# Optimization experiments

Hardware: AMD Instinct MI355X
Metric: run time of the kernel (lower is better)

The kernel has to match this reference:

```python
import jax, jax.numpy as jnp
import numpy as np

N, E, B = 20000, 160000, 64
NFEAT, NHID, HEADS, NCLASS = 128, 64, 16, 10
GAT_SLOPE = 0.2    # LeakyReLU inside GATv2 attention
OUT_SLOPE = 0.01   # torch.nn.functional.leaky_relu default
TEMPERATURE = 1.0


def _lrelu(x, slope):
    return jnp.where(x >= 0, x, slope * x)


def gatv2_conv(x, src, dst, Wl, bl, Wr, br, att, bias):
    # x: [N, Fin]; PyG GATv2Conv with share_weights=False, concat=False (mean over heads)
    xl = (x @ Wl + bl).reshape(N, HEADS, NHID)   # source-side transform
    xr = (x @ Wr + br).reshape(N, HEADS, NHID)   # target-side transform
    e = _lrelu(xl[src] + xr[dst], GAT_SLOPE)     # [E', H, C] per-edge pre-activation
    logit = jnp.einsum('ehc,hc->eh', e, att)     # [E', H]
    # segment softmax over incoming edges of each target node (self-loops guarantee >=1 edge)
    m = jax.ops.segment_max(logit, dst, num_segments=N)
    m = jnp.where(jnp.isfinite(m), m, 0.0)
    ex = jnp.exp(logit - m[dst])
    den = jax.ops.segment_sum(ex, dst, num_segments=N)
    alpha = ex / den[dst]                        # [E', H]
    out = jax.ops.segment_sum(alpha[:, :, None] * xl[src], dst, num_segments=N)  # [N, H, C]
    return out.mean(axis=1) + bias               # concat=False -> head average, then bias


def setup_inputs() -> dict:
    key = jax.random.key(0)
    ks = jax.random.split(key, 20)
    s = 0.05
    inp = {
        'x': jax.random.normal(ks[0], (N, NFEAT), dtype=jnp.float32),
        'edge_index': jax.random.randint(ks[1], (2, E), 0, N, dtype=jnp.int64)
            if jax.config.jax_enable_x64 else jax.random.randint(ks[1], (2, E), 0, N).astype(jnp.int32),
        'batch': jnp.sort(jax.random.randint(ks[2], (N,), 0, B)).astype(jnp.int32),
        # GATv2 layer 1
        'W1l': jax.random.normal(ks[3], (NFEAT, HEADS * NHID), dtype=jnp.float32) * s,
        'b1l': jnp.zeros((HEADS * NHID,), jnp.float32),
        'W1r': jax.random.normal(ks[4], (NFEAT, HEADS * NHID), dtype=jnp.float32) * s,
        'b1r': jnp.zeros((HEADS * NHID,), jnp.float32),
        'att1': jax.random.normal(ks[5], (HEADS, NHID), dtype=jnp.float32) * s,
        'bias1': jnp.zeros((NHID,), jnp.float32),
        # GATv2 layer 2
        'W2l': jax.random.normal(ks[6], (NHID, HEADS * NHID), dtype=jnp.float32) * s,
        'b2l': jnp.zeros((HEADS * NHID,), jnp.float32),
        'W2r': jax.random.normal(ks[7], (NHID, HEADS * NHID), dtype=jnp.float32) * s,
        'b2r': jnp.zeros((HEADS * NHID,), jnp.float32),
        'att2': jax.random.normal(ks[8], (HEADS, NHID), dtype=jnp.float32) * s,
        'bias2': jnp.zeros((NHID,), jnp.float32),
        # heads
        'Wc': jax.random.normal(ks[9], (NHID, NCLASS), dtype=jnp.float32) * s,
        'bc': jnp.zeros((NCLASS,), jnp.float32),
        'Wv': jax.random.normal(ks[10], (NHID, 1), dtype=jnp.float32) * s,
        'bv': jnp.zeros((1,), jnp.float32),
    }
    return inp


def reference(x, edge_index, batch, W1l, b1l, W1r, b1r, att1, bias1,
              W2l, b2l, W2r, b2r, att2, bias2, Wc, bc, Wv, bv):
    loop = jnp.arange(N, dtype=edge_index.dtype)  # PyG add_self_loops=True
    src = jnp.concatenate([edge_index[0], loop])
    dst = jnp.concatenate([edge_index[1], loop])

    h = _lrelu(gatv2_conv(x, src, dst, W1l, b1l, W1r, b1r, att1, bias1), OUT_SLOPE)
    h = _lrelu(gatv2_conv(h, src, dst, W2l, b2l, W2r, b2r, att2, bias2), OUT_SLOPE)
    # dropout p=0.0 -> identity

    sums = jax.ops.segment_sum(h, batch, num_segments=B)           # [B, NHID]
    cnt = jax.ops.segment_sum(jnp.ones((N,), h.dtype), batch, num_segments=B)
    pooled = sums / jnp.maximum(cnt, 1.0)[:, None]                 # global_mean_pool

    logits = (pooled @ Wc + bc) / TEMPERATURE                      # [B, NCLASS]
    log_var = pooled @ Wv + bv                                     # [B, 1]
    return (logits, log_var)
```

## Files before the change

### kernel.cpp

```cpp
#include <hip/hip_runtime.h>
#include <hip/hip_bf16.h>
#include <hip/hip_fp16.h>
#include <math.h>

#define NN   20000
#define EE   160000
#define NBAT 64
#define NF   128
#define NH   64
#define NHEAD 16
#define NCLS 10
#define ETOT (EE + NN)

typedef __attribute__((ext_vector_type(8))) short short8;
typedef __attribute__((ext_vector_type(8))) _Float16 half8;
typedef __attribute__((ext_vector_type(4))) float f32x4;
typedef unsigned short ushort_t;

static __device__ __forceinline__ ushort_t f2bf_rn(float x) {
    unsigned u = __builtin_bit_cast(unsigned, x);
    unsigned r = (u + 0x7fffu + ((u >> 16) & 1u)) >> 16;
    return (ushort_t)r;
}
static __device__ __forceinline__ float bf2f(ushort_t u) {
    unsigned v = (unsigned)u << 16;
    return __builtin_bit_cast(float, v);
}

__global__ void k_init_deg(int* __restrict__ deg) {
    int n = blockIdx.x * 256 + threadIdx.x;
    if (n < NN) deg[n] = 1;
}

__global__ void k_hist(const int* __restrict__ ei, int* __restrict__ deg) {
    int e = blockIdx.x * 256 + threadIdx.x;
    if (e < EE) atomicAdd(&deg[ei[EE + e]], 1);
}

__global__ void k_scan(const int* __restrict__ deg, int* __restrict__ rowptr,
                       int* __restrict__ cursor) {
    const int T = 1024, PER = (NN + T - 1) / T;
    __shared__ int part[T];
    int t = threadIdx.x;
    int local[PER];
    int s = 0;
    #pragma unroll
    for (int i = 0; i < PER; ++i) {
        int idx = t * PER + i;
        int v = (idx < NN) ? deg[idx] : 0;
        local[i] = v; s += v;
    }
    part[t] = s;
    __syncthreads();
    for (int off = 1; off < T; off <<= 1) {
        int v = (t >= off) ? part[t - off] : 0;
        __syncthreads();
        part[t] += v;
        __syncthreads();
    }
    int ex = (t == 0) ? 0 : part[t - 1];
    #pragma unroll
    for (int i = 0; i < PER; ++i) {
        int idx = t * PER + i;
        if (idx < NN) { rowptr[idx] = ex; cursor[idx] = ex; ex += local[i]; }
    }
    if (t == T - 1) rowptr[NN] = ex;
}

__global__ void k_scatter(const int* __restrict__ ei, int* __restrict__ cursor,
                          int* __restrict__ csr) {
    int e = blockIdx.x * 256 + threadIdx.x;
    if (e >= ETOT) return;
    int s, d;
    if (e < EE) { s = ei[e]; d = ei[EE + e]; }
    else        { s = e - EE; d = s; }
    int pos = atomicAdd(&cursor[d], 1);
    csr[pos] = s;
}

__global__ void k_bounds(const int* __restrict__ batch, int* __restrict__ bstart) {
    int n = blockIdx.x * 256 + threadIdx.x;
    if (n >= NN) return;
    int b = batch[n];
    if (n == 0) for (int bb = 0; bb <= b; ++bb) bstart[bb] = 0;
    int bn = (n + 1 < NN) ? batch[n + 1] : NBAT;
    for (int bb = b + 1; bb <= bn; ++bb) bstart[bb] = n + 1;
}

__global__ void k_split_a(const float* __restrict__ A, ushort_t* __restrict__ hi,
                          ushort_t* __restrict__ lo, int count4) {
    int idx = blockIdx.x * 256 + threadIdx.x;
    if (idx >= count4) return;
    float4 x = *(const float4*)(A + idx * 4);
    ushort4 h, l;
    h.x = f2bf_rn(x.x); l.x = f2bf_rn(x.x - bf2f(h.x));
    h.y = f2bf_rn(x.y); l.y = f2bf_rn(x.y - bf2f(h.y));
    h.z = f2bf_rn(x.z); l.z = f2bf_rn(x.z - bf2f(h.z));
    h.w = f2bf_rn(x.w); l.w = f2bf_rn(x.w - bf2f(h.w));
    *(ushort4*)(hi + idx * 4) = h;
    *(ushort4*)(lo + idx * 4) = l;
}

template<int K>
__global__ void k_split_w(const float* __restrict__ W, ushort_t* __restrict__ hi,
                          ushort_t* __restrict__ lo) {
    int idx = blockIdx.x * 256 + threadIdx.x;
    if (idx >= K * 1024) return;
    int k = idx >> 10, n = idx & 1023;
    float x = W[idx];
    ushort_t h = f2bf_rn(x);
    hi[n * K + k] = h;
    lo[n * K + k] = f2bf_rn(x - bf2f(h));
}

template<int K>
__global__ __launch_bounds__(256) void k_gemm_mfma(
    const ushort_t* __restrict__ Ahi, const ushort_t* __restrict__ Alo, int M,
    const ushort_t* __restrict__ W0hi, const ushort_t* __restrict__ W0lo,
    const float* __restrict__ b0, _Float16* __restrict__ O0,
    const ushort_t* __restrict__ W1hi, const ushort_t* __restrict__ W1lo,
    const float* __restrict__ b1, _Float16* __restrict__ O1)
{
    const ushort_t* Whi = blockIdx.z ? W1hi : W0hi;
    const ushort_t* Wlo = blockIdx.z ? W1lo : W0lo;
    const float*    bi  = blockIdx.z ? b1 : b0;
    _Float16*       O   = blockIdx.z ? O1 : O0;

    const int r0 = blockIdx.x * 128;
    const int c0 = blockIdx.y * 128;

    __shared__ __align__(16) ushort_t As_hi[128 * 64];
    __shared__ __align__(16) ushort_t As_lo[128 * 64];
    __shared__ __align__(16) ushort_t Ws_hi[128 * 64];
    __shared__ __align__(16) ushort_t Ws_lo[128 * 64];

    const int t = threadIdx.x;
    const int lane = t & 63;
    const int wv = t >> 6, wr = wv >> 1, wc = wv & 1;
    const int fr = lane & 15;
    const int k0 = (lane >> 4) * 8;

    f32x4 acc[4][4] = {};

    for (int kt = 0; kt < K; kt += 64) {
        #pragma unroll
        for (int p = 0; p < 4; ++p) {
            int idx = p * 256 + t;
            int m  = idx >> 3;
            int kc = (idx & 7) * 8;
            int gr = r0 + m;
            uint4 vh = make_uint4(0, 0, 0, 0), vl = make_uint4(0, 0, 0, 0);
            if (gr < M) {
                vh = *(const uint4*)(Ahi + (size_t)gr * K + kt + kc);
                vl = *(const uint4*)(Alo + (size_t)gr * K + kt + kc);
            }
            int sw = (m * 128 + kc * 2) ^ ((m & 7) << 4);
            *(uint4*)((char*)As_hi + sw) = vh;
            *(uint4*)((char*)As_lo + sw) = vl;
            uint4 wh = *(const uint4*)(Whi + (size_t)(c0 + m) * K + kt + kc);
            uint4 wl = *(const uint4*)(Wlo + (size_t)(c0 + m) * K + kt + kc);
            *(uint4*)((char*)Ws_hi + sw) = wh;
            *(uint4*)((char*)Ws_lo + sw) = wl;
        }
        __syncthreads();

        #pragma unroll
        for (int ks = 0; ks < 64; ks += 32) {
            short8 ah[4], al[4], bh[4], bl[4];
            #pragma unroll
            for (int i = 0; i < 4; ++i) {
                int row = wr * 64 + i * 16 + fr;
                int off = (row * 128 + (ks + k0) * 2) ^ ((row & 7) << 4);
                ah[i] = *(const short8*)((const char*)As_hi + off);
                al[i] = *(const short8*)((const char*)As_lo + off);
            }
            #pragma unroll
            for (int j = 0; j < 4; ++j) {
                int col = wc * 64 + j * 16 + fr;
                int off = (col * 128 + (ks + k0) * 2) ^ ((col & 7) << 4);
                bh[j] = *(const short8*)((const char*)Ws_hi + off);
                bl[j] = *(const short8*)((const char*)Ws_lo + off);
            }
            #pragma unroll
            for (int i = 0; i < 4; ++i)
                #pragma unroll
                for (int j = 0; j < 4; ++j) {
                    acc[i][j] = __builtin_amdgcn_mfma_f32_16x16x32_bf16(ah[i], bh[j], acc[i][j], 0, 0, 0);
                    acc[i][j] = __builtin_amdgcn_mfma_f32_16x16x32_bf16(ah[i], bl[j], acc[i][j], 0, 0, 0);
                    acc[i][j] = __builtin_amdgcn_mfma_f32_16x16x32_bf16(al[i], bh[j], acc[i][j], 0, 0, 0);
                }
        }
        __syncthreads();
    }

    float bj[4];
    #pragma unroll
    for (int j = 0; j < 4; ++j) bj[j] = bi[c0 + wc * 64 + j * 16 + fr];
    #pragma unroll
    for (int i = 0; i < 4; ++i) {
        int rbase = r0 + wr * 64 + i * 16 + (lane >> 4) * 4;
        #pragma unroll
        for (int r = 0; r < 4; ++r) {
            int gr = rbase + r;
            if (gr < M) {
                #pragma unroll
                for (int j = 0; j < 4; ++j)
                    O[(size_t)gr * 1024 + c0 + wc * 64 + j * 16 + fr] =
                        (_Float16)(acc[i][j][r] + bj[j]);
            }
        }
    }
}

template<int SPLIT>
__global__ __launch_bounds__(256) void k_attn(
    const _Float16* __restrict__ xl, const _Float16* __restrict__ xr,
    const float* __restrict__ att, const float* __restrict__ bias,
    const int* __restrict__ rowptr, const int* __restrict__ csr,
    float* __restrict__ hout, ushort_t* __restrict__ hhi, ushort_t* __restrict__ hlo)
{
    const int wave = threadIdx.x >> 6;
    const int lane = threadIdx.x & 63;
    const int n = blockIdx.x * 4 + wave;
    if (n >= NN) return;
    const int h  = lane >> 2;
    const int cc = lane & 3;
    const int cb = h * NH + cc * 16;

    float attv[16], xrv[16], acc[16];
    #pragma unroll
    for (int i = 0; i < 4; ++i)
        *(float4*)(attv + i * 4) = *(const float4*)(att + cb + i * 4);
    {
        half8 q0 = *(const half8*)(xr + (size_t)n * 1024 + cb);
        half8 q1 = *(const half8*)(xr + (size_t)n * 1024 + cb + 8);
        #pragma unroll
        for (int j = 0; j < 8; ++j) { xrv[j] = (float)q0[j]; xrv[8 + j] = (float)q1[j]; }
    }
    #pragma unroll
    for (int j = 0; j < 16; ++j) acc[j] = 0.f;

    float m = -INFINITY, den = 0.f;
    const int e0 = rowptr[n], e1 = rowptr[n + 1];
    int e = e0;

    for (; e + 2 <= e1; e += 2) {
        const int s0 = csr[e], s1 = csr[e + 1];
        const _Float16* p0 = xl + (size_t)s0 * 1024 + cb;
        const _Float16* p1 = xl + (size_t)s1 * 1024 + cb;
        half8 a0 = *(const half8*)p0;
        half8 a1 = *(const half8*)(p0 + 8);
        half8 b0 = *(const half8*)p1;
        half8 b1 = *(const half8*)(p1 + 8);
        float x0[16], x1[16];
        #pragma unroll
        for (int j = 0; j < 8; ++j) {
            x0[j] = (float)a0[j]; x0[8 + j] = (float)a1[j];
            x1[j] = (float)b0[j]; x1[8 + j] = (float)b1[j];
        }
        float l0 = 0.f, l1 = 0.f;
        #pragma unroll
        for (int j = 0; j < 16; ++j) {
            float t0 = x0[j] + xrv[j];
            float t1 = x1[j] + xrv[j];
            t0 = fmaxf(t0, 0.2f * t0);
            t1 = fmaxf(t1, 0.2f * t1);
            l0 = fmaf(t0, attv[j], l0);
            l1 = fmaf(t1, attv[j], l1);
        }
        l0 += __shfl_xor(l0, 1); l1 += __shfl_xor(l1, 1);
        l0 += __shfl_xor(l0, 2); l1 += __shfl_xor(l1, 2);
        {
            const float nm = fmaxf(m, l0);
            const float p  = __expf(l0 - nm);
            const float sc = __expf(m - nm);
            den = den * sc + p;
            #pragma unroll
            for (int j = 0; j < 16; ++j) acc[j] = fmaf(acc[j], sc, p * x0[j]);
            m = nm;
        }
        {
            const float nm = fmaxf(m, l1);
            const float p  = __expf(l1 - nm);
            const float sc = __expf(m - nm);
            den = den * sc + p;
            #pragma unroll
            for (int j = 0; j < 16; ++j) acc[j] = fmaf(acc[j], sc, p * x1[j]);
            m = nm;
        }
    }
    for (; e < e1; ++e) {
        const int s = csr[e];
        const _Float16* p0 = xl + (size_t)s * 1024 + cb;
        half8 a0 = *(const half8*)p0;
        half8 a1 = *(const half8*)(p0 + 8);
        float x0[16];
        #pragma unroll
        for (int j = 0; j < 8; ++j) { x0[j] = (float)a0[j]; x0[8 + j] = (float)a1[j]; }
        float l0 = 0.f;
        #pragma unroll
        for (int j = 0; j < 16; ++j) {
            float t0 = x0[j] + xrv[j];
            t0 = fmaxf(t0, 0.2f * t0);
            l0 = fmaf(t0, attv[j], l0);
        }
        l0 += __shfl_xor(l0, 1);
        l0 += __shfl_xor(l0, 2);
        const float nm = fmaxf(m, l0);
        const float p  = __expf(l0 - nm);
        const float sc = __expf(m - nm);
        den = den * sc + p;
        #pragma unroll
        for (int j = 0; j < 16; ++j) acc[j] = fmaf(acc[j], sc, p * x0[j]);
        m = nm;
    }

    const float inv = 1.f / den;
    float v[16];
    #pragma unroll
    for (int j = 0; j < 16; ++j) v[j] = acc[j] * inv;
    #pragma unroll
    for (int mask = 4; mask <= 32; mask <<= 1)
        #pragma unroll
        for (int j = 0; j < 16; ++j) v[j] += __shfl_xor(v[j], mask);

    if (h == 0) {
        float bvv[16];
        #pragma unroll
        for (int i = 0; i < 4; ++i)
            *(float4*)(bvv + i * 4) = *(const float4*)(bias + cc * 16 + i * 4);
        #pragma unroll
        for (int i = 0; i < 4; ++i) {
            float o[4];
            #pragma unroll
            for (int r = 0; r < 4; ++r) {
                float tt = v[i * 4 + r] * 0.0625f + bvv[i * 4 + r];
                o[r] = fmaxf(tt, 0.01f * tt);
            }
            if (SPLIT) {
                ushort4 hh, ll;
                hh.x = f2bf_rn(o[0]); ll.x = f2bf_rn(o[0] - bf2f(hh.x));
                hh.y = f2bf_rn(o[1]); ll.y = f2bf_rn(o[1] - bf2f(hh.y));
                hh.z = f2bf_rn(o[2]); ll.z = f2bf_rn(o[2] - bf2f(hh.z));
                hh.w = f2bf_rn(o[3]); ll.w = f2bf_rn(o[3] - bf2f(hh.w));
                *(ushort4*)(hhi + (size_t)n * NH + cc * 16 + i * 4) = hh;
                *(ushort4*)(hlo + (size_t)n * NH + cc * 16 + i * 4) = ll;
            } else {
                *(float4*)(hout + (size_t)n * NH + cc * 16 + i * 4) =
                    make_float4(o[0], o[1], o[2], o[3]);
            }
        }
    }
}

#define PNODES 128
__global__ __launch_bounds__(256) void k_pool_partial(
    const float* __restrict__ h2, const int* __restrict__ batch,
    float* __restrict__ sums)
{
    const int n0 = blockIdx.x * PNODES;
    const int c = threadIdx.x & 63;
    const int r = threadIdx.x >> 6;
    const int nend = (n0 + PNODES < NN) ? n0 + PNODES : NN;
    float s = 0.f;
    int bcur = -1;
    for (int n = n0 + r; n < nend; n += 4) {
        int b = batch[n];
        if (b != bcur) {
            if (bcur >= 0) atomicAdd(&sums[bcur * NH + c], s);
            bcur = b; s = 0.f;
        }
        s += h2[(size_t)n * NH + c];
    }
    if (bcur >= 0) atomicAdd(&sums[bcur * NH + c], s);
}

__global__ void k_heads(const float* __restrict__ sums, const int* __restrict__ bstart,
                        const float* __restrict__ Wc, const float* __restrict__ bc,
                        const float* __restrict__ Wv, const float* __restrict__ bv,
                        float* __restrict__ out)
{
    const int b = blockIdx.x, c = threadIdx.x;
    const float cnt = (float)(bstart[b + 1] - bstart[b]);
    const float pooled = sums[b * NH + c] / fmaxf(cnt, 1.f);
    __shared__ float pl[NH];
    pl[c] = pooled;
    __syncthreads();
    if (c < NCLS) {
        float a = bc[c];
        for (int k = 0; k < NH; ++k) a = fmaf(pl[k], Wc[k * NCLS + c], a);
        out[b * NCLS + c] = a;
    } else if (c == NCLS) {
        float a = bv[0];
        for (int k = 0; k < NH; ++k) a = fmaf(pl[k], Wv[k], a);
        out[NBAT * NCLS + b] = a;
    }
}

extern "C" void kernel_launch(void* const* d_in, const int* in_sizes, int n_in,
                              void* d_out, int out_size, void* d_ws, size_t ws_size,
                              hipStream_t stream)
{
    const float* x     = (const float*)d_in[0];
    const int*   ei    = (const int*)  d_in[1];
    const int*   batch = (const int*)  d_in[2];
    const float* W1l = (const float*)d_in[3],  *b1l = (const float*)d_in[4];
    const float* W1r = (const float*)d_in[5],  *b1r = (const float*)d_in[6];
    const float* att1 = (const float*)d_in[7], *bias1 = (const float*)d_in[8];
    const float* W2l = (const float*)d_in[9],  *b2l = (const float*)d_in[10];
    const float* W2r = (const float*)d_in[11], *b2r = (const float*)d_in[12];
    const float* att2 = (const float*)d_in[13], *bias2 = (const float*)d_in[14];
    const float* Wc = (const float*)d_in[15],  *bc = (const float*)d_in[16];
    const float* Wv = (const float*)d_in[17],  *bv = (const float*)d_in[18];
    float* out = (float*)d_out;

    char* ws = (char*)d_ws;
    size_t off = 0;
    auto carve = [&](size_t bytes) {
        char* p = ws + off;
        off = (off + bytes + 255) & ~(size_t)255;
        return p;
    };
    _Float16* xl    = (_Float16*)carve((size_t)NN * 1024 * 2);
    _Float16* xr    = (_Float16*)carve((size_t)NN * 1024 * 2);
    float*    h2    = (float*)carve((size_t)NN * NH * 4);
    float*    psums = (float*)carve((size_t)NBAT * NH * 4);
    ushort_t* Axhi  = (ushort_t*)carve((size_t)NN * NF * 2);
    ushort_t* Axlo  = (ushort_t*)carve((size_t)NN * NF * 2);
    ushort_t* h1hi  = (ushort_t*)carve((size_t)NN * NH * 2);
    ushort_t* h1lo  = (ushort_t*)carve((size_t)NN * NH * 2);
    ushort_t* Wt1lh = (ushort_t*)carve((size_t)1024 * NF * 2);
    ushort_t* Wt1ll = (ushort_t*)carve((size_t)1024 * NF * 2);
    ushort_t* Wt1rh = (ushort_t*)carve((size_t)1024 * NF * 2);
    ushort_t* Wt1rl = (ushort_t*)carve((size_t)1024 * NF * 2);
    ushort_t* Wt2lh = (ushort_t*)carve((size_t)1024 * NH * 2);
    ushort_t* Wt2ll = (ushort_t*)carve((size_t)1024 * NH * 2);
    ushort_t* Wt2rh = (ushort_t*)carve((size_t)1024 * NH * 2);
    ushort_t* Wt2rl = (ushort_t*)carve((size_t)1024 * NH * 2);
    int*      deg    = (int*)carve((size_t)NN * 4);
    int*      cursor = (int*)carve((size_t)NN * 4);
    int*      rowptr = (int*)carve((size_t)(NN + 1) * 4);
    int*      csr    = (int*)carve((size_t)ETOT * 4);
    int*      bstart = (int*)carve((size_t)(NBAT + 1) * 4);

    k_init_deg<<<(NN + 255) / 256, 256, 0, stream>>>(deg);
    k_hist   <<<(EE + 255) / 256, 256, 0, stream>>>(ei, deg);
    k_scan   <<<1, 1024, 0, stream>>>(deg, rowptr, cursor);
    k_scatter<<<(ETOT + 255) / 256, 256, 0, stream>>>(ei, cursor, csr);
    k_bounds <<<(NN + 255) / 256, 256, 0, stream>>>(batch, bstart);

    k_split_a<<<(NN * NF / 4 + 255) / 256, 256, 0, stream>>>(x, Axhi, Axlo, NN * NF / 4);
    k_split_w<NF><<<(NF * 1024 + 255) / 256, 256, 0, stream>>>(W1l, Wt1lh, Wt1ll);
    k_split_w<NF><<<(NF * 1024 + 255) / 256, 256, 0, stream>>>(W1r, Wt1rh, Wt1rl);
    k_split_w<NH><<<(NH * 1024 + 255) / 256, 256, 0, stream>>>(W2l, Wt2lh, Wt2ll);
    k_split_w<NH><<<(NH * 1024 + 255) / 256, 256, 0, stream>>>(W2r, Wt2rh, Wt2rl);

    const int MB = (NN + 127) / 128;
    k_gemm_mfma<NF><<<dim3(MB, 8, 2), 256, 0, stream>>>(
        Axhi, Axlo, NN, Wt1lh, Wt1ll, b1l, xl, Wt1rh, Wt1rl, b1r, xr);
    k_attn<1><<<NN / 4, 256, 0, stream>>>(xl, xr, att1, bias1, rowptr, csr,
                                          (float*)nullptr, h1hi, h1lo);
    k_gemm_mfma<NH><<<dim3(MB, 8, 2), 256, 0, stream>>>(
        h1hi, h1lo, NN, Wt2lh, Wt2ll, b2l, xl, Wt2rh, Wt2rl, b2r, xr);
    k_attn<0><<<NN / 4, 256, 0, stream>>>(xl, xr, att2, bias2, rowptr, csr,
                                          h2, (ushort_t*)nullptr, (ushort_t*)nullptr);
    hipMemsetAsync(psums, 0, (size_t)NBAT * NH * 4, stream);
    k_pool_partial<<<(NN + PNODES - 1) / PNODES, 256, 0, stream>>>(h2, batch, psums);
    k_heads<<<NBAT, NH, 0, stream>>>(psums, bstart, Wc, bc, Wv, bv, out);
}
```

Baseline: 387.1 us.

## Use packed fp16 dot2 in attention, unroll edges by four, restructure CSR build

The attention logit is now computed in packed fp16 (add, leaky-relu, fdot2 against fp16 attention weights) instead of converting every gathered element to fp32. The edge loop is unrolled to four gathers per iteration so more loads are in flight. Self-loops are written directly in the scan kernel, and the degree init kernel is replaced by a memset. The GEMM grid is swapped so column tiles vary fastest, which may improve reuse of the A tile in cache. The fp16 arithmetic lowers logit precision, which risks accuracy drift.

```diff
diff --git a/kernel.cpp b/kernel.cpp
--- a/kernel.cpp
+++ b/kernel.cpp
@@ -14,8 +14,21 @@
 
 typedef __attribute__((ext_vector_type(8))) short short8;
 typedef __attribute__((ext_vector_type(8))) _Float16 half8;
+typedef __attribute__((ext_vector_type(2))) _Float16 h2;
 typedef __attribute__((ext_vector_type(4))) float f32x4;
 typedef unsigned short ushort_t;
+
+#if __has_builtin(__builtin_amdgcn_fdot2)
+typedef __fp16 fdot2_t __attribute__((ext_vector_type(2)));
+static __device__ __forceinline__ float dot2(h2 a, h2 b, float c) {
+    return __builtin_amdgcn_fdot2(__builtin_bit_cast(fdot2_t, a),
+                                  __builtin_bit_cast(fdot2_t, b), c, false);
+}
+#else
+static __device__ __forceinline__ float dot2(h2 a, h2 b, float c) {
+    return c + (float)a.x * (float)b.x + (float)a.y * (float)b.y;
+}
+#endif
 
 static __device__ __forceinline__ ushort_t f2bf_rn(float x) {
     unsigned u = __builtin_bit_cast(unsigned, x);
@@ -27,18 +40,13 @@
     return __builtin_bit_cast(float, v);
 }
 
-__global__ void k_init_deg(int* __restrict__ deg) {
-    int n = blockIdx.x * 256 + threadIdx.x;
-    if (n < NN) deg[n] = 1;
-}
-
 __global__ void k_hist(const int* __restrict__ ei, int* __restrict__ deg) {
     int e = blockIdx.x * 256 + threadIdx.x;
     if (e < EE) atomicAdd(&deg[ei[EE + e]], 1);
 }
 
 __global__ void k_scan(const int* __restrict__ deg, int* __restrict__ rowptr,
-                       int* __restrict__ cursor) {
+                       int* __restrict__ cursor, int* __restrict__ csr) {
     const int T = 1024, PER = (NN + T - 1) / T;
     __shared__ int part[T];
     int t = threadIdx.x;
@@ -62,18 +70,22 @@
     #pragma unroll
     for (int i = 0; i < PER; ++i) {
         int idx = t * PER + i;
-        if (idx < NN) { rowptr[idx] = ex; cursor[idx] = ex; ex += local[i]; }
-    }
-    if (t == T - 1) rowptr[NN] = ex;
+        if (idx < NN) {
+            int base = ex + idx;
+            rowptr[idx] = base;
+            csr[base]   = idx;
+            cursor[idx] = base + 1;
+            ex += local[i];
+        }
+    }
+    if (t == T - 1) rowptr[NN] = ex + NN;
 }
 
 __global__ void k_scatter(const int* __restrict__ ei, int* __restrict__ cursor,
                           int* __restrict__ csr) {
     int e = blockIdx.x * 256 + threadIdx.x;
-    if (e >= ETOT) return;
-    int s, d;
-    if (e < EE) { s = ei[e]; d = ei[EE + e]; }
-    else        { s = e - EE; d = s; }
+    if (e >= EE) return;
+    int s = ei[e], d = ei[EE + e];
     int pos = atomicAdd(&cursor[d], 1);
     csr[pos] = s;
 }
@@ -126,8 +138,8 @@
     const float*    bi  = blockIdx.z ? b1 : b0;
     _Float16*       O   = blockIdx.z ? O1 : O0;
 
-    const int r0 = blockIdx.x * 128;
-    const int c0 = blockIdx.y * 128;
+    const int c0 = blockIdx.x * 128;
+    const int r0 = blockIdx.y * 128;
 
     __shared__ __align__(16) ushort_t As_hi[128 * 64];
     __shared__ __align__(16) ushort_t As_lo[128 * 64];
@@ -212,6 +224,36 @@
     }
 }
 
+static __device__ __forceinline__ void edge_update(
+    half8 a0, half8 a1, half8 xr0, half8 xr1, const h2* att2,
+    float& m, float& den, float* acc)
+{
+    half8 t0 = a0 + xr0;
+    half8 t1 = a1 + xr1;
+    t0 = __builtin_elementwise_max(t0, t0 * (_Float16)0.2f);
+    t1 = __builtin_elementwise_max(t1, t1 * (_Float16)0.2f);
+    const h2* p0 = (const h2*)&t0;
+    const h2* p1 = (const h2*)&t1;
+    float lg = 0.f;
+    #pragma unroll
+    for (int j = 0; j < 4; ++j) lg = dot2(p0[j], att2[j], lg);
+    #pragma unroll
+    for (int j = 0; j < 4; ++j) lg = dot2(p1[j], att2[4 + j], lg);
+    lg += __shfl_xor(lg, 1);
+    lg += __shfl_xor(lg, 2);
+    const float nm = fmaxf(m, lg);
+    const float p  = __expf(lg - nm);
+    const float sc = __expf(m - nm);
+    den = den * sc + p;
+    const _Float16* xa = (const _Float16*)&a0;
+    const _Float16* xb = (const _Float16*)&a1;
+    #pragma unroll
+    for (int j = 0; j < 8; ++j) acc[j]     = fmaf((float)xa[j], p, acc[j] * sc);
+    #pragma unroll
+    for (int j = 0; j < 8; ++j) acc[8 + j] = fmaf((float)xb[j], p, acc[8 + j] * sc);
+    m = nm;
+}
+
 template<int SPLIT>
 __global__ __launch_bounds__(256) void k_attn(
     const _Float16* __restrict__ xl, const _Float16* __restrict__ xr,
@@ -227,92 +269,43 @@
     const int cc = lane & 3;
     const int cb = h * NH + cc * 16;
 
-    float attv[16], xrv[16], acc[16];
-    #pragma unroll
-    for (int i = 0; i < 4; ++i)
-        *(float4*)(attv + i * 4) = *(const float4*)(att + cb + i * 4);
-    {
-        half8 q0 = *(const half8*)(xr + (size_t)n * 1024 + cb);
-        half8 q1 = *(const half8*)(xr + (size_t)n * 1024 + cb + 8);
-        #pragma unroll
-        for (int j = 0; j < 8; ++j) { xrv[j] = (float)q0[j]; xrv[8 + j] = (float)q1[j]; }
-    }
+    h2 att2[8];
+    #pragma unroll
+    for (int i = 0; i < 4; ++i) {
+        float4 a = *(const float4*)(att + cb + i * 4);
+        att2[i * 2 + 0] = h2{(_Float16)a.x, (_Float16)a.y};
+        att2[i * 2 + 1] = h2{(_Float16)a.z, (_Float16)a.w};
+    }
+    const half8 xr0 = *(const half8*)(xr + (size_t)n * 1024 + cb);
+    const half8 xr1 = *(const half8*)(xr + (size_t)n * 1024 + cb + 8);
+
+    float acc[16];
     #pragma unroll
     for (int j = 0; j < 16; ++j) acc[j] = 0.f;
-
     float m = -INFINITY, den = 0.f;
+
     const int e0 = rowptr[n], e1 = rowptr[n + 1];
     int e = e0;
-
-    for (; e + 2 <= e1; e += 2) {
-        const int s0 = csr[e], s1 = csr[e + 1];
+    for (; e + 4 <= e1; e += 4) {
+        const int s0 = csr[e], s1 = csr[e + 1], s2 = csr[e + 2], s3 = csr[e + 3];
         const _Float16* p0 = xl + (size_t)s0 * 1024 + cb;
         const _Float16* p1 = xl + (size_t)s1 * 1024 + cb;
-        half8 a0 = *(const half8*)p0;
-        half8 a1 = *(const half8*)(p0 + 8);
-        half8 b0 = *(const half8*)p1;
-        half8 b1 = *(const half8*)(p1 + 8);
-        float x0[16], x1[16];
-        #pragma unroll
-        for (int j = 0; j < 8; ++j) {
-            x0[j] = (float)a0[j]; x0[8 + j] = (float)a1[j];
-            x1[j] = (float)b0[j]; x1[8 + j] = (float)b1[j];
-        }
-        float l0 = 0.f, l1 = 0.f;
-        #pragma unroll
-        for (int j = 0; j < 16; ++j) {
-            float t0 = x0[j] + xrv[j];
-            float t1 = x1[j] + xrv[j];
-            t0 = fmaxf(t0, 0.2f * t0);
-            t1 = fmaxf(t1, 0.2f * t1);
-            l0 = fmaf(t0, attv[j], l0);
-            l1 = fmaf(t1, attv[j], l1);
-        }
-        l0 += __shfl_xor(l0, 1); l1 += __shfl_xor(l1, 1);
-        l0 += __shfl_xor(l0, 2); l1 += __shfl_xor(l1, 2);
-        {
-            const float nm = fmaxf(m, l0);
-            const float p  = __expf(l0 - nm);
-            const float sc = __expf(m - nm);
-            den = den * sc + p;
-            #pragma unroll
-            for (int j = 0; j < 16; ++j) acc[j] = fmaf(acc[j], sc, p * x0[j]);
-            m = nm;
-        }
-        {
-            const float nm = fmaxf(m, l1);
-            const float p  = __expf(l1 - nm);
-            const float sc = __expf(m - nm);
-            den = den * sc + p;
-            #pragma unroll
-            for (int j = 0; j < 16; ++j) acc[j] = fmaf(acc[j], sc, p * x1[j]);
-            m = nm;
-        }
+        const _Float16* p2 = xl + (size_t)s2 * 1024 + cb;
+        const _Float16* p3 = xl + (size_t)s3 * 1024 + cb;
+        half8 a0 = *(const half8*)p0, a1 = *(const half8*)(p0 + 8);
+        half8 b0 = *(const half8*)p1, b1 = *(const half8*)(p1 + 8);
+        half8 c0 = *(const half8*)p2, c1 = *(const half8*)(p2 + 8);
+        half8 d0 = *(const half8*)p3, d1 = *(const half8*)(p3 + 8);
+        edge_update(a0, a1, xr0, xr1, att2, m, den, acc);
+        edge_update(b0, b1, xr0, xr1, att2, m, den, acc);
+        edge_update(c0, c1, xr0, xr1, att2, m, den, acc);
+        edge_update(d0, d1, xr0, xr1, att2, m, den, acc);
     }
     for (; e < e1; ++e) {
         const int s = csr[e];
         const _Float16* p0 = xl + (size_t)s * 1024 + cb;
-        half8 a0 = *(const half8*)p0;
-        half8 a1 = *(const half8*)(p0 + 8);
-        float x0[16];
-        #pragma unroll
-        for (int j = 0; j < 8; ++j) { x0[j] = (float)a0[j]; x0[8 + j] = (float)a1[j]; }
-        float l0 = 0.f;
-        #pragma unroll
-        for (int j = 0; j < 16; ++j) {
-            float t0 = x0[j] + xrv[j];
-            t0 = fmaxf(t0, 0.2f * t0);
-            l0 = fmaf(t0, attv[j], l0);
-        }
-        l0 += __shfl_xor(l0, 1);
-        l0 += __shfl_xor(l0, 2);
-        const float nm = fmaxf(m, l0);
-        const float p  = __expf(l0 - nm);
-        const float sc = __expf(m - nm);
-        den = den * sc + p;
-        #pragma unroll
-        for (int j = 0; j < 16; ++j) acc[j] = fmaf(acc[j], sc, p * x0[j]);
-        m = nm;
+        half8 a0 = *(const half8*)p0, a1 = *(const half8*)(p0 + 8);
+        edge_update(a0, a1, xr0, xr1, att2, m, den, acc);
     }
 
     const float inv = 1.f / den;
@@ -355,7 +348,7 @@
 
 #define PNODES 128
 __global__ __launch_bounds__(256) void k_pool_partial(
-    const float* __restrict__ h2, const int* __restrict__ batch,
+    const float* __restrict__ h2buf, const int* __restrict__ batch,
     float* __restrict__ sums)
 {
     const int n0 = blockIdx.x * PNODES;
@@ -370,7 +363,7 @@
             if (bcur >= 0) atomicAdd(&sums[bcur * NH + c], s);
             bcur = b; s = 0.f;
         }
-        s += h2[(size_t)n * NH + c];
+        s += h2buf[(size_t)n * NH + c];
     }
     if (bcur >= 0) atomicAdd(&sums[bcur * NH + c], s);
 }
@@ -423,7 +416,7 @@
     };
     _Float16* xl    = (_Float16*)carve((size_t)NN * 1024 * 2);
     _Float16* xr    = (_Float16*)carve((size_t)NN * 1024 * 2);
-    float*    h2    = (float*)carve((size_t)NN * NH * 4);
+    float*    h2b   = (float*)carve((size_t)NN * NH * 4);
     float*    psums = (float*)carve((size_t)NBAT * NH * 4);
     ushort_t* Axhi  = (ushort_t*)carve((size_t)NN * NF * 2);
     ushort_t* Axlo  = (ushort_t*)carve((size_t)NN * NF * 2);
@@ -443,10 +436,10 @@
     int*      csr    = (int*)carve((size_t)ETOT * 4);
     int*      bstart = (int*)carve((size_t)(NBAT + 1) * 4);
 
-    k_init_deg<<<(NN + 255) / 256, 256, 0, stream>>>(deg);
+    hipMemsetAsync(deg, 0, (size_t)NN * 4, stream);
     k_hist   <<<(EE + 255) / 256, 256, 0, stream>>>(ei, deg);
-    k_scan   <<<1, 1024, 0, stream>>>(deg, rowptr, cursor);
-    k_scatter<<<(ETOT + 255) / 256, 256, 0, stream>>>(ei, cursor, csr);
+    k_scan   <<<1, 1024, 0, stream>>>(deg, rowptr, cursor, csr);
+    k_scatter<<<(EE + 255) / 256, 256, 0, stream>>>(ei, cursor, csr);
     k_bounds <<<(NN + 255) / 256, 256, 0, stream>>>(batch, bstart);
 
     k_split_a<<<(NN * NF / 4 + 255) / 256, 256, 0, stream>>>(x, Axhi, Axlo, NN * NF / 4);
@@ -456,15 +449,15 @@
     k_split_w<NH><<<(NH * 1024 + 255) / 256, 256, 0, stream>>>(W2r, Wt2rh, Wt2rl);
 
     const int MB = (NN + 127) / 128;
-    k_gemm_mfma<NF><<<dim3(MB, 8, 2), 256, 0, stream>>>(
+    k_gemm_mfma<NF><<<dim3(8, MB, 2), 256, 0, stream>>>(
         Axhi, Axlo, NN, Wt1lh, Wt1ll, b1l, xl, Wt1rh, Wt1rl, b1r, xr);
     k_attn<1><<<NN / 4, 256, 0, stream>>>(xl, xr, att1, bias1, rowptr, csr,
                                           (float*)nullptr, h1hi, h1lo);
-    k_gemm_mfma<NH><<<dim3(MB, 8, 2), 256, 0, stream>>>(
+    k_gemm_mfma<NH><<<dim3(8, MB, 2), 256, 0, stream>>>(
         h1hi, h1lo, NN, Wt2lh, Wt2ll, b2l, xl, Wt2rh, Wt2rl, b2r, xr);
     k_attn<0><<<NN / 4, 256, 0, stream>>>(xl, xr, att2, bias2, rowptr, csr,
-                                          h2, (ushort_t*)nullptr, (ushort_t*)nullptr);
+                                          h2b, (ushort_t*)nullptr, (ushort_t*)nullptr);
     hipMemsetAsync(psums, 0, (size_t)NBAT * NH * 4, stream);
-    k_pool_partial<<<(NN + PNODES - 1) / PNODES, 256, 0, stream>>>(h2, batch, psums);
+    k_pool_partial<<<(NN + PNODES - 1) / PNODES, 256, 0, stream>>>(h2b, batch, psums);
     k_heads<<<NBAT, NH, 0, stream>>>(psums, bstart, Wc, bc, Wv, bv, out);
 }
```

After: 394.4 us. About the same (+1.9%).
